# Performance work log

Measured on AMD Instinct MI355X. Metric: run time of the kernel, lower is better.

## Reference

```python
import jax, jax.numpy as jnp
import numpy as np
from jax import lax

DIM = 384
NUM_HEADS = 12
HEAD_DIM = DIM // NUM_HEADS
SCALE = HEAD_DIM ** -0.5


def setup_inputs() -> dict:
    key = jax.random.key(0)
    ks = jax.random.split(key, 7)
    B, H, W = 8, 32, 32
    s = 0.02
    return {
        "x": jax.random.normal(ks[0], (B, DIM, H, W), jnp.float32),
        "qkvo_w": jax.random.normal(ks[1], (4 * DIM, DIM, 1, 1), jnp.float32) * s,
        "qkvo_b": jax.random.normal(ks[2], (4 * DIM,), jnp.float32) * s,
        "lepe_w": jax.random.normal(ks[3], (DIM, 1, 5, 5), jnp.float32) * s,
        "lepe_b": jax.random.normal(ks[4], (DIM,), jnp.float32) * s,
        "proj_w": jax.random.normal(ks[5], (DIM, DIM, 1, 1), jnp.float32) * s,
        "proj_b": jax.random.normal(ks[6], (DIM,), jnp.float32) * s,
    }


def reference(x, qkvo_w, qkvo_b, lepe_w, lepe_b, proj_w, proj_b):
    B, C, H, W = x.shape
    n, d = NUM_HEADS, HEAD_DIM
    HW = H * W

    # fused 1x1 QKVO projection: [B, 4C, H, W]
    qkvo = jnp.einsum('oc,bchw->bohw', qkvo_w[:, :, 0, 0], x) + qkvo_b[:, None, None]
    qkv = qkvo[:, :3 * C]
    o = qkvo[:, 3 * C:]

    # depthwise 5x5 LePE on v channels
    v_ch = qkv[:, 2 * C:]
    lepe = lax.conv_general_dilated(
        v_ch, lepe_w, window_strides=(1, 1), padding='SAME',
        feature_group_count=C,
        dimension_numbers=('NCHW', 'OIHW', 'NCHW')) + lepe_b[:, None, None]

    # split heads: channels ordered (m n d) -> q,k,v each [B, n, HW, d]
    q, k, v = jnp.transpose(qkv.reshape(B, 3, n, d, HW), (1, 0, 2, 4, 3))

    attn = jax.nn.softmax(SCALE * jnp.einsum('bnqd,bnkd->bnqk', q, k), axis=-1)
    res = jnp.einsum('bnqk,bnkd->bnqd', attn, v)  # [B, n, HW, d]
    res = jnp.transpose(res, (0, 1, 3, 2)).reshape(B, C, H, W)

    res = res + lepe
    out = jnp.einsum('oc,bchw->bohw', proj_w[:, :, 0, 0], res * o) + proj_b[:, None, None]
    return out
```

## Files before the change

### kernel.cpp

```cpp
#include <hip/hip_runtime.h>
#include <hip/hip_bf16.h>

#define DIM   384
#define NH    12
#define HD    32
#define HWSZ  1024
#define BATCH 8
#define SCALE 0.17677669529663687f
#define EXP_K (SCALE * 1.4426950408889634f)

typedef __attribute__((ext_vector_type(8))) short bf16x8;
typedef __attribute__((ext_vector_type(4))) float floatx4;

__device__ __forceinline__ unsigned short f2bf(float x) {
    union { __hip_bfloat16 h; unsigned short u; } c;
    c.h = __float2bfloat16(x);
    return c.u;
}
__device__ __forceinline__ float bf2f(unsigned short h) {
    union { unsigned int u; float f; } v; v.u = ((unsigned int)h) << 16;
    return v.f;
}

__global__ __launch_bounds__(256) void cast_w(
    const float* __restrict__ wa, const float* __restrict__ wb,
    unsigned short* __restrict__ da, unsigned short* __restrict__ db, int na8)
{
    const int idx = blockIdx.x * 256 + threadIdx.x;
    const float* src; unsigned short* dst; int i;
    if (idx < na8) { src = wa; dst = da; i = idx; }
    else           { src = wb; dst = db; i = idx - na8; }
    float4 f0 = *(const float4*)&src[i * 8];
    float4 f1 = *(const float4*)&src[i * 8 + 4];
    ushort4 h0 = make_ushort4(f2bf(f0.x), f2bf(f0.y), f2bf(f0.z), f2bf(f0.w));
    ushort4 h1 = make_ushort4(f2bf(f1.x), f2bf(f1.y), f2bf(f1.z), f2bf(f1.w));
    *(ushort4*)&dst[i * 8] = h0;
    *(ushort4*)&dst[i * 8 + 4] = h1;
}

__global__ __launch_bounds__(256) void tcast_f32(
    const float* __restrict__ in, unsigned short* __restrict__ out, int C, int N)
{
    __shared__ __align__(16) unsigned short t[32][36];
    const int n0 = blockIdx.x * 32, c0 = blockIdx.y * 32, b = blockIdx.z;
    const float* ib = in + (size_t)b * C * N;
    unsigned short* ob = out + (size_t)b * N * C;
    const int tid = threadIdx.x;
    const int r = tid >> 3, q = (tid & 7) * 4;
    float4 f = *(const float4*)&ib[(size_t)(c0 + r) * N + n0 + q];
    ushort4 h = make_ushort4(f2bf(f.x), f2bf(f.y), f2bf(f.z), f2bf(f.w));
    *(ushort4*)&t[r][q] = h;
    __syncthreads();
    ushort4 o;
    o.x = t[q + 0][r]; o.y = t[q + 1][r]; o.z = t[q + 2][r]; o.w = t[q + 3][r];
    *(ushort4*)&ob[(size_t)(n0 + r) * C + c0 + q] = o;
}

__global__ __launch_bounds__(256) void tcast_b16(
    const unsigned short* __restrict__ in, unsigned short* __restrict__ out, int C, int N)
{
    __shared__ __align__(16) unsigned short t[32][36];
    const int n0 = blockIdx.x * 32, c0 = blockIdx.y * 32, b = blockIdx.z;
    const unsigned short* ib = in + (size_t)b * C * N;
    unsigned short* ob = out + (size_t)b * N * C;
    const int tid = threadIdx.x;
    const int r = tid >> 3, q = (tid & 7) * 4;
    ushort4 h = *(const ushort4*)&ib[(size_t)(c0 + r) * N + n0 + q];
    *(ushort4*)&t[r][q] = h;
    __syncthreads();
    ushort4 o;
    o.x = t[q + 0][r]; o.y = t[q + 1][r]; o.z = t[q + 2][r]; o.w = t[q + 3][r];
    *(ushort4*)&ob[(size_t)(n0 + r) * C + c0 + q] = o;
}

template<int MODE>
__global__ __launch_bounds__(256) void gemm_mfma(
    const unsigned short* __restrict__ Wb16, const unsigned short* __restrict__ Xt,
    const float* __restrict__ bias, unsigned short* __restrict__ qkT,
    unsigned short* __restrict__ vo, float* __restrict__ Yf,
    int M, int K, int N)
{
    __shared__ __align__(16) unsigned short As[64][72];
    __shared__ __align__(16) unsigned short Bs[64][72];

    const int b = blockIdx.z, m0 = blockIdx.y * 64, n0 = blockIdx.x * 64;
    const int tid = threadIdx.x;
    const int w = tid >> 6, lane = tid & 63;
    const int g = lane >> 4, c = lane & 15;

    const unsigned short* Xb = Xt + (size_t)b * N * K;

    floatx4 acc[4];
    #pragma unroll
    for (int nb = 0; nb < 4; ++nb) acc[nb] = (floatx4){0.f, 0.f, 0.f, 0.f};

    const int row = tid >> 2, cq = (tid & 3) * 16;

    for (int k0 = 0; k0 < K; k0 += 64) {
        __syncthreads();
        {
            const unsigned short* wp = &Wb16[(size_t)(m0 + row) * K + k0 + cq];
            *(bf16x8*)&As[row][cq]     = *(const bf16x8*)wp;
            *(bf16x8*)&As[row][cq + 8] = *(const bf16x8*)(wp + 8);
            const unsigned short* xp = &Xb[(size_t)(n0 + row) * K + k0 + cq];
            *(bf16x8*)&Bs[row][cq]     = *(const bf16x8*)xp;
            *(bf16x8*)&Bs[row][cq + 8] = *(const bf16x8*)(xp + 8);
        }
        __syncthreads();

        bf16x8 af0 = *(const bf16x8*)&As[16 * w + c][8 * g];
        bf16x8 af1 = *(const bf16x8*)&As[16 * w + c][32 + 8 * g];
        #pragma unroll
        for (int nb = 0; nb < 4; ++nb) {
            bf16x8 bf0 = *(const bf16x8*)&Bs[nb * 16 + c][8 * g];
            bf16x8 bf1 = *(const bf16x8*)&Bs[nb * 16 + c][32 + 8 * g];
            acc[nb] = __builtin_amdgcn_mfma_f32_16x16x32_bf16(af0, bf0, acc[nb], 0, 0, 0);
            acc[nb] = __builtin_amdgcn_mfma_f32_16x16x32_bf16(af1, bf1, acc[nb], 0, 0, 0);
        }
    }

    const int mbase = m0 + 16 * w + 4 * g;
    float bi[4];
    #pragma unroll
    for (int r = 0; r < 4; ++r) bi[r] = bias[mbase + r];

    if (MODE == 0) {
        if (m0 < 768) {
            const float qs = (m0 < 384) ? EXP_K : 1.0f;
            #pragma unroll
            for (int nb = 0; nb < 4; ++nb) {
                const int n = n0 + nb * 16 + c;
                ushort4 h;
                h.x = f2bf((acc[nb][0] + bi[0]) * qs);
                h.y = f2bf((acc[nb][1] + bi[1]) * qs);
                h.z = f2bf((acc[nb][2] + bi[2]) * qs);
                h.w = f2bf((acc[nb][3] + bi[3]) * qs);
                *(ushort4*)&qkT[((size_t)b * HWSZ + n) * 768 + mbase] = h;
            }
        } else {
            #pragma unroll
            for (int nb = 0; nb < 4; ++nb) {
                const int n = n0 + nb * 16 + c;
                #pragma unroll
                for (int r = 0; r < 4; ++r)
                    vo[((size_t)b * 768 + (mbase - 768 + r)) * HWSZ + n] =
                        f2bf(acc[nb][r] + bi[r]);
            }
        }
    } else {
        #pragma unroll
        for (int nb = 0; nb < 4; ++nb) {
            const int n = n0 + nb * 16 + c;
            #pragma unroll
            for (int r = 0; r < 4; ++r)
                Yf[((size_t)b * M + mbase + r) * (size_t)N + n] = acc[nb][r] + bi[r];
        }
    }
}

__global__ __launch_bounds__(512) void attn_mfma(
    const unsigned short* __restrict__ qkT, const unsigned short* __restrict__ vo,
    unsigned short* __restrict__ res)
{
    __shared__ __align__(16) unsigned short Ks[64][40];
    __shared__ __align__(16) unsigned short Vs[32][72];
    __shared__ __align__(16) unsigned short Ps[128][72];
    __shared__ float lbuf[128];

    const int b = blockIdx.z, h = blockIdx.y, p0 = blockIdx.x * 128;
    const int tid = threadIdx.x;
    const int w = tid >> 6, lane = tid & 63;
    const int g = lane >> 4, c = lane & 15;

    const unsigned short* qkTb = qkT + (size_t)b * HWSZ * 768;
    const unsigned short* vb   = vo + ((size_t)b * 768 + h * HD) * HWSZ;

    bf16x8 qf = *(const bf16x8*)&qkTb[(size_t)(p0 + 16 * w + c) * 768 + h * HD + 8 * g];

    floatx4 oacc0 = (floatx4){0.f, 0.f, 0.f, 0.f};
    floatx4 oacc1 = (floatx4){0.f, 0.f, 0.f, 0.f};
    float Lacc = 0.f;

    for (int j0 = 0; j0 < HWSZ; j0 += 64) {
        __syncthreads();
        if (tid < 256) {
            const int jr = tid >> 2, d8 = (tid & 3) * 8;
            *(bf16x8*)&Ks[jr][d8] =
                *(const bf16x8*)&qkTb[(size_t)(j0 + jr) * 768 + 384 + h * HD + d8];
        } else {
            const int t = tid - 256;
            const int dr = t >> 3, j8 = (t & 7) * 8;
            *(bf16x8*)&Vs[dr][j8] =
                *(const bf16x8*)&vb[(size_t)dr * HWSZ + j0 + j8];
        }
        __syncthreads();

        #pragma unroll
        for (int jb = 0; jb < 4; ++jb) {
            bf16x8 kf = *(const bf16x8*)&Ks[jb * 16 + c][8 * g];
            floatx4 st = (floatx4){0.f, 0.f, 0.f, 0.f};
            st = __builtin_amdgcn_mfma_f32_16x16x32_bf16(kf, qf, st, 0, 0, 0);
            float e0 = exp2f(st[0]);
            float e1 = exp2f(st[1]);
            float e2 = exp2f(st[2]);
            float e3 = exp2f(st[3]);
            Lacc += (e0 + e1) + (e2 + e3);
            ushort4 pe = make_ushort4(f2bf(e0), f2bf(e1), f2bf(e2), f2bf(e3));
            *(ushort4*)&Ps[16 * w + c][jb * 16 + 4 * g] = pe;
        }

        #pragma unroll
        for (int jk = 0; jk < 2; ++jk) {
            bf16x8 pf  = *(const bf16x8*)&Ps[16 * w + c][jk * 32 + 8 * g];
            bf16x8 vf0 = *(const bf16x8*)&Vs[c][jk * 32 + 8 * g];
            bf16x8 vf1 = *(const bf16x8*)&Vs[16 + c][jk * 32 + 8 * g];
            oacc0 = __builtin_amdgcn_mfma_f32_16x16x32_bf16(pf, vf0, oacc0, 0, 0, 0);
            oacc1 = __builtin_amdgcn_mfma_f32_16x16x32_bf16(pf, vf1, oacc1, 0, 0, 0);
        }
    }

    Lacc += __shfl_xor(Lacc, 16, 64);
    Lacc += __shfl_xor(Lacc, 32, 64);
    if (g == 0) lbuf[16 * w + c] = Lacc;

    float linv[4];
    #pragma unroll
    for (int r = 0; r < 4; ++r) linv[r] = 1.0f / lbuf[16 * w + 4 * g + r];

    unsigned short* rp = res + ((size_t)b * DIM + h * HD) * HWSZ;
    const int pbase = p0 + 16 * w + 4 * g;
    ushort4 h0, h1;
    h0.x = f2bf(oacc0[0] * linv[0]); h0.y = f2bf(oacc0[1] * linv[1]);
    h0.z = f2bf(oacc0[2] * linv[2]); h0.w = f2bf(oacc0[3] * linv[3]);
    h1.x = f2bf(oacc1[0] * linv[0]); h1.y = f2bf(oacc1[1] * linv[1]);
    h1.z = f2bf(oacc1[2] * linv[2]); h1.w = f2bf(oacc1[3] * linv[3]);
    *(ushort4*)&rp[(size_t)c * HWSZ + pbase] = h0;
    *(ushort4*)&rp[(size_t)(16 + c) * HWSZ + pbase] = h1;
}

__global__ __launch_bounds__(256) void lepe_mul(
    const unsigned short* __restrict__ vo, const float* __restrict__ lw,
    const float* __restrict__ lb, const unsigned short* __restrict__ res,
    unsigned short* __restrict__ gated)
{
    const int cch = blockIdx.x, b = blockIdx.y;
    const unsigned short* v  = vo + ((size_t)b * 768 + cch) * HWSZ;
    const unsigned short* o  = vo + ((size_t)b * 768 + 384 + cch) * HWSZ;
    const unsigned short* rp = res + ((size_t)b * DIM + cch) * HWSZ;
    unsigned short* gp = gated + ((size_t)b * DIM + cch) * HWSZ;

    __shared__ float vs[1024];
    __shared__ float wgt[25];

    const int tid = threadIdx.x;
    {
        ushort4 hv = *(const ushort4*)&v[tid * 4];
        vs[tid * 4 + 0] = bf2f(hv.x); vs[tid * 4 + 1] = bf2f(hv.y);
        vs[tid * 4 + 2] = bf2f(hv.z); vs[tid * 4 + 3] = bf2f(hv.w);
    }
    if (tid < 25) wgt[tid] = lw[cch * 25 + tid];
    __syncthreads();

    const float bias = lb[cch];
    const int q0 = tid * 4;
    const int y  = q0 >> 5;
    const int x0 = q0 & 31;

    float acc[4] = {bias, bias, bias, bias};
    #pragma unroll
    for (int ky = 0; ky < 5; ++ky) {
        int iy = y + ky - 2;
        if ((unsigned)iy < 32u) {
            #pragma unroll
            for (int kx = 0; kx < 5; ++kx) {
                float wv = wgt[ky * 5 + kx];
                #pragma unroll
                for (int u = 0; u < 4; ++u) {
                    int ix = x0 + u + kx - 2;
                    if ((unsigned)ix < 32u) acc[u] += wv * vs[iy * 32 + ix];
                }
            }
        }
    }

    ushort4 rh = *(const ushort4*)&rp[q0];
    ushort4 oh = *(const ushort4*)&o[q0];
    ushort4 outv;
    outv.x = f2bf((bf2f(rh.x) + acc[0]) * bf2f(oh.x));
    outv.y = f2bf((bf2f(rh.y) + acc[1]) * bf2f(oh.y));
    outv.z = f2bf((bf2f(rh.z) + acc[2]) * bf2f(oh.z));
    outv.w = f2bf((bf2f(rh.w) + acc[3]) * bf2f(oh.w));
    *(ushort4*)&gp[q0] = outv;
}

extern "C" void kernel_launch(void* const* d_in, const int* in_sizes, int n_in,
                              void* d_out, int out_size, void* d_ws, size_t ws_size,
                              hipStream_t stream)
{
    const float* x      = (const float*)d_in[0];
    const float* qkvo_w = (const float*)d_in[1];
    const float* qkvo_b = (const float*)d_in[2];
    const float* lepe_w = (const float*)d_in[3];
    const float* lepe_b = (const float*)d_in[4];
    const float* proj_w = (const float*)d_in[5];
    const float* proj_b = (const float*)d_in[6];

    unsigned short* xt     = (unsigned short*)d_ws;
    unsigned short* qkT    = xt     + (size_t)BATCH * HWSZ * DIM;
    unsigned short* vo     = qkT    + (size_t)BATCH * HWSZ * 768;
    unsigned short* res    = vo     + (size_t)BATCH * 768 * HWSZ;
    unsigned short* gated  = res    + (size_t)BATCH * DIM * HWSZ;
    unsigned short* gatedT = gated  + (size_t)BATCH * DIM * HWSZ;
    unsigned short* wqb    = gatedT + (size_t)BATCH * HWSZ * DIM;
    unsigned short* wpb    = wqb    + (size_t)1536 * DIM;

    cast_w<<<dim3((73728 + 18432) / 256), 256, 0, stream>>>(
        qkvo_w, proj_w, wqb, wpb, 73728);

    tcast_f32<<<dim3(32, 12, BATCH), 256, 0, stream>>>(x, xt, DIM, HWSZ);

    gemm_mfma<0><<<dim3(16, 24, BATCH), 256, 0, stream>>>(
        wqb, xt, qkvo_b, qkT, vo, nullptr, 4 * DIM, DIM, HWSZ);

    attn_mfma<<<dim3(8, NH, BATCH), 512, 0, stream>>>(qkT, vo, res);

    lepe_mul<<<dim3(DIM, BATCH), 256, 0, stream>>>(vo, lepe_w, lepe_b, res, gated);

    tcast_b16<<<dim3(32, 12, BATCH), 256, 0, stream>>>(gated, gatedT, DIM, HWSZ);

    gemm_mfma<1><<<dim3(16, 6, BATCH), 256, 0, stream>>>(
        wpb, gatedT, proj_b, nullptr, nullptr, (float*)d_out, DIM, DIM, HWSZ);
}
```

Baseline: 173.0 us.

## Enlarge GEMM tiles to 128x128 and read K/V directly from global in attention

The projection GEMMs now use 128x128 block tiles with each warp computing a 64x64 sub-tile via 16 MFMA accumulators, which raises operand reuse per LDS load. The attention kernel drops LDS staging of K and V and the per-iteration barriers, loading fragments straight from global/cache. Block indices are remapped so consecutive blocks share the same batch-head and can reuse K/V in L2. Risks are fewer GEMM blocks (lower occupancy), higher register pressure, and exposed global-load latency in attention.

```diff
diff --git a/kernel.cpp b/kernel.cpp
--- a/kernel.cpp
+++ b/kernel.cpp
@@ -80,80 +80,90 @@
     unsigned short* __restrict__ vo, float* __restrict__ Yf,
     int M, int K, int N)
 {
-    __shared__ __align__(16) unsigned short As[64][72];
-    __shared__ __align__(16) unsigned short Bs[64][72];
-
-    const int b = blockIdx.z, m0 = blockIdx.y * 64, n0 = blockIdx.x * 64;
+    __shared__ __align__(16) unsigned short As[128][40];
+    __shared__ __align__(16) unsigned short Bs[128][40];
+
+    const int b = blockIdx.z, m0 = blockIdx.y * 128, n0 = blockIdx.x * 128;
     const int tid = threadIdx.x;
     const int w = tid >> 6, lane = tid & 63;
+    const int wr = w >> 1, wc = w & 1;
     const int g = lane >> 4, c = lane & 15;
 
     const unsigned short* Xb = Xt + (size_t)b * N * K;
 
-    floatx4 acc[4];
+    floatx4 acc[4][4];
     #pragma unroll
-    for (int nb = 0; nb < 4; ++nb) acc[nb] = (floatx4){0.f, 0.f, 0.f, 0.f};
-
-    const int row = tid >> 2, cq = (tid & 3) * 16;
-
-    for (int k0 = 0; k0 < K; k0 += 64) {
+    for (int i = 0; i < 4; ++i)
+        #pragma unroll
+        for (int j = 0; j < 4; ++j) acc[i][j] = (floatx4){0.f, 0.f, 0.f, 0.f};
+
+    const int srow = tid >> 1, shh = (tid & 1) * 16;
+
+    for (int k0 = 0; k0 < K; k0 += 32) {
         __syncthreads();
         {
-            const unsigned short* wp = &Wb16[(size_t)(m0 + row) * K + k0 + cq];
-            *(bf16x8*)&As[row][cq]     = *(const bf16x8*)wp;
-            *(bf16x8*)&As[row][cq + 8] = *(const bf16x8*)(wp + 8);
-            const unsigned short* xp = &Xb[(size_t)(n0 + row) * K + k0 + cq];
-            *(bf16x8*)&Bs[row][cq]     = *(const bf16x8*)xp;
-            *(bf16x8*)&Bs[row][cq + 8] = *(const bf16x8*)(xp + 8);
+            const unsigned short* wp = &Wb16[(size_t)(m0 + srow) * K + k0 + shh];
+            *(bf16x8*)&As[srow][shh]     = *(const bf16x8*)wp;
+            *(bf16x8*)&As[srow][shh + 8] = *(const bf16x8*)(wp + 8);
+            const unsigned short* xp = &Xb[(size_t)(n0 + srow) * K + k0 + shh];
+            *(bf16x8*)&Bs[srow][shh]     = *(const bf16x8*)xp;
+            *(bf16x8*)&Bs[srow][shh + 8] = *(const bf16x8*)(xp + 8);
         }
         __syncthreads();
 
-        bf16x8 af0 = *(const bf16x8*)&As[16 * w + c][8 * g];
-        bf16x8 af1 = *(const bf16x8*)&As[16 * w + c][32 + 8 * g];
-        #pragma unroll
-        for (int nb = 0; nb < 4; ++nb) {
-            bf16x8 bf0 = *(const bf16x8*)&Bs[nb * 16 + c][8 * g];
-            bf16x8 bf1 = *(const bf16x8*)&Bs[nb * 16 + c][32 + 8 * g];
-            acc[nb] = __builtin_amdgcn_mfma_f32_16x16x32_bf16(af0, bf0, acc[nb], 0, 0, 0);
-            acc[nb] = __builtin_amdgcn_mfma_f32_16x16x32_bf16(af1, bf1, acc[nb], 0, 0, 0);
-        }
-    }
-
-    const int mbase = m0 + 16 * w + 4 * g;
-    float bi[4];
+        bf16x8 af[4], bfj[4];
+        #pragma unroll
+        for (int i = 0; i < 4; ++i)
+            af[i] = *(const bf16x8*)&As[64 * wr + 16 * i + c][8 * g];
+        #pragma unroll
+        for (int j = 0; j < 4; ++j)
+            bfj[j] = *(const bf16x8*)&Bs[64 * wc + 16 * j + c][8 * g];
+        #pragma unroll
+        for (int i = 0; i < 4; ++i)
+            #pragma unroll
+            for (int j = 0; j < 4; ++j)
+                acc[i][j] = __builtin_amdgcn_mfma_f32_16x16x32_bf16(
+                    af[i], bfj[j], acc[i][j], 0, 0, 0);
+    }
+
     #pragma unroll
-    for (int r = 0; r < 4; ++r) bi[r] = bias[mbase + r];
-
-    if (MODE == 0) {
-        if (m0 < 768) {
-            const float qs = (m0 < 384) ? EXP_K : 1.0f;
-            #pragma unroll
-            for (int nb = 0; nb < 4; ++nb) {
-                const int n = n0 + nb * 16 + c;
-                ushort4 h;
-                h.x = f2bf((acc[nb][0] + bi[0]) * qs);
-                h.y = f2bf((acc[nb][1] + bi[1]) * qs);
-                h.z = f2bf((acc[nb][2] + bi[2]) * qs);
-                h.w = f2bf((acc[nb][3] + bi[3]) * qs);
-                *(ushort4*)&qkT[((size_t)b * HWSZ + n) * 768 + mbase] = h;
+    for (int i = 0; i < 4; ++i) {
+        const int m = m0 + 64 * wr + 16 * i + 4 * g;
+        float bi[4];
+        #pragma unroll
+        for (int r = 0; r < 4; ++r) bi[r] = bias[m + r];
+
+        if (MODE == 0) {
+            if (m0 < 768) {
+                const float qs = (m0 < 384) ? EXP_K : 1.0f;
+                #pragma unroll
+                for (int j = 0; j < 4; ++j) {
+                    const int n = n0 + 64 * wc + 16 * j + c;
+                    ushort4 h;
+                    h.x = f2bf((acc[i][j][0] + bi[0]) * qs);
+                    h.y = f2bf((acc[i][j][1] + bi[1]) * qs);
+                    h.z = f2bf((acc[i][j][2] + bi[2]) * qs);
+                    h.w = f2bf((acc[i][j][3] + bi[3]) * qs);
+                    *(ushort4*)&qkT[((size_t)b * HWSZ + n) * 768 + m] = h;
+                }
+            } else {
+                #pragma unroll
+                for (int j = 0; j < 4; ++j) {
+                    const int n = n0 + 64 * wc + 16 * j + c;
+                    #pragma unroll
+                    for (int r = 0; r < 4; ++r)
+                        vo[((size_t)b * 768 + (m - 768 + r)) * HWSZ + n] =
+                            f2bf(acc[i][j][r] + bi[r]);
+                }
             }
         } else {
             #pragma unroll
-            for (int nb = 0; nb < 4; ++nb) {
-                const int n = n0 + nb * 16 + c;
+            for (int j = 0; j < 4; ++j) {
+                const int n = n0 + 64 * wc + 16 * j + c;
                 #pragma unroll
                 for (int r = 0; r < 4; ++r)
-                    vo[((size_t)b * 768 + (mbase - 768 + r)) * HWSZ + n] =
-                        f2bf(acc[nb][r] + bi[r]);
+                    Yf[((size_t)b * M + m + r) * (size_t)N + n] = acc[i][j][r] + bi[r];
             }
-        }
-    } else {
-        #pragma unroll
-        for (int nb = 0; nb < 4; ++nb) {
-            const int n = n0 + nb * 16 + c;
-            #pragma unroll
-            for (int r = 0; r < 4; ++r)
-                Yf[((size_t)b * M + mbase + r) * (size_t)N + n] = acc[nb][r] + bi[r];
         }
     }
 }
@@ -162,17 +172,20 @@
     const unsigned short* __restrict__ qkT, const unsigned short* __restrict__ vo,
     unsigned short* __restrict__ res)
 {
-    __shared__ __align__(16) unsigned short Ks[64][40];
-    __shared__ __align__(16) unsigned short Vs[32][72];
     __shared__ __align__(16) unsigned short Ps[128][72];
     __shared__ float lbuf[128];
 
-    const int b = blockIdx.z, h = blockIdx.y, p0 = blockIdx.x * 128;
+    const int gidx = blockIdx.x * 96 + blockIdx.y + 12 * blockIdx.z;
+    const int bh = gidx >> 3, pblk = gidx & 7;
+    const int b = bh / 12, h = bh % 12;
+    const int p0 = pblk * 128;
+
     const int tid = threadIdx.x;
     const int w = tid >> 6, lane = tid & 63;
     const int g = lane >> 4, c = lane & 15;
 
     const unsigned short* qkTb = qkT + (size_t)b * HWSZ * 768;
+    const unsigned short* kb   = qkTb + 384 + h * HD;
     const unsigned short* vb   = vo + ((size_t)b * 768 + h * HD) * HWSZ;
 
     bf16x8 qf = *(const bf16x8*)&qkTb[(size_t)(p0 + 16 * w + c) * 768 + h * HD + 8 * g];
@@ -182,22 +195,9 @@
     float Lacc = 0.f;
 
     for (int j0 = 0; j0 < HWSZ; j0 += 64) {
-        __syncthreads();
-        if (tid < 256) {
-            const int jr = tid >> 2, d8 = (tid & 3) * 8;
-            *(bf16x8*)&Ks[jr][d8] =
-                *(const bf16x8*)&qkTb[(size_t)(j0 + jr) * 768 + 384 + h * HD + d8];
-        } else {
-            const int t = tid - 256;
-            const int dr = t >> 3, j8 = (t & 7) * 8;
-            *(bf16x8*)&Vs[dr][j8] =
-                *(const bf16x8*)&vb[(size_t)dr * HWSZ + j0 + j8];
-        }
-        __syncthreads();
-
         #pragma unroll
         for (int jb = 0; jb < 4; ++jb) {
-            bf16x8 kf = *(const bf16x8*)&Ks[jb * 16 + c][8 * g];
+            bf16x8 kf = *(const bf16x8*)&kb[(size_t)(j0 + jb * 16 + c) * 768 + 8 * g];
             floatx4 st = (floatx4){0.f, 0.f, 0.f, 0.f};
             st = __builtin_amdgcn_mfma_f32_16x16x32_bf16(kf, qf, st, 0, 0, 0);
             float e0 = exp2f(st[0]);
@@ -212,8 +212,8 @@
         #pragma unroll
         for (int jk = 0; jk < 2; ++jk) {
             bf16x8 pf  = *(const bf16x8*)&Ps[16 * w + c][jk * 32 + 8 * g];
-            bf16x8 vf0 = *(const bf16x8*)&Vs[c][jk * 32 + 8 * g];
-            bf16x8 vf1 = *(const bf16x8*)&Vs[16 + c][jk * 32 + 8 * g];
+            bf16x8 vf0 = *(const bf16x8*)&vb[(size_t)c * HWSZ + j0 + jk * 32 + 8 * g];
+            bf16x8 vf1 = *(const bf16x8*)&vb[(size_t)(16 + c) * HWSZ + j0 + jk * 32 + 8 * g];
             oacc0 = __builtin_amdgcn_mfma_f32_16x16x32_bf16(pf, vf0, oacc0, 0, 0, 0);
             oacc1 = __builtin_amdgcn_mfma_f32_16x16x32_bf16(pf, vf1, oacc1, 0, 0, 0);
         }
@@ -319,7 +319,7 @@
 
     tcast_f32<<<dim3(32, 12, BATCH), 256, 0, stream>>>(x, xt, DIM, HWSZ);
 
-    gemm_mfma<0><<<dim3(16, 24, BATCH), 256, 0, stream>>>(
+    gemm_mfma<0><<<dim3(8, 12, BATCH), 256, 0, stream>>>(
         wqb, xt, qkvo_b, qkT, vo, nullptr, 4 * DIM, DIM, HWSZ);
 
     attn_mfma<<<dim3(8, NH, BATCH), 512, 0, stream>>>(qkT, vo, res);
@@ -328,6 +328,6 @@
 
     tcast_b16<<<dim3(32, 12, BATCH), 256, 0, stream>>>(gated, gatedT, DIM, HWSZ);
 
-    gemm_mfma<1><<<dim3(16, 6, BATCH), 256, 0, stream>>>(
+    gemm_mfma<1><<<dim3(8, 3, BATCH), 256, 0, stream>>>(
         wpb, gatedT, proj_b, nullptr, nullptr, (float*)d_out, DIM, DIM, HWSZ);
 }
```

Measured after the change: 216.6 us. +25.2%, slower.
